# Kernel optimization log

Measured on AMD Instinct MI355X. Metric: run time of the kernel, lower is better.

The kernel has to match this reference:

```python
import jax, jax.numpy as jnp
import numpy as np

B, S, D = 1, 2048, 4096
H, KV = 32, 8
HD = D // H          # 128
N_REP = H // KV      # 4
ROPE_THETA = 10000.0


def setup_inputs() -> dict:
    key = jax.random.key(0)
    ks = jax.random.split(key, 5)
    x = jax.random.normal(ks[0], (B, S, D), dtype=jnp.float32)
    wq = jax.random.normal(ks[1], (H * HD, D), dtype=jnp.float32) * 0.02
    wk = jax.random.normal(ks[2], (KV * HD, D), dtype=jnp.float32) * 0.02
    wv = jax.random.normal(ks[3], (KV * HD, D), dtype=jnp.float32) * 0.02
    wo = jax.random.normal(ks[4], (D, H * HD), dtype=jnp.float32) * 0.02
    # precomputed RoPE frequencies: freqs_cis = exp(i * t * theta_j)
    inv_freq = 1.0 / (ROPE_THETA ** (np.arange(0, HD, 2, dtype=np.float32) / HD))  # [HD/2]
    angles = np.arange(S, dtype=np.float32)[:, None] * inv_freq[None, :]           # [S, HD/2]
    freqs_cos = jnp.asarray(np.cos(angles))
    freqs_sin = jnp.asarray(np.sin(angles))
    return {"x": x, "freqs_cos": freqs_cos, "freqs_sin": freqs_sin,
            "wq": wq, "wk": wk, "wv": wv, "wo": wo}


def _rope(t, cos, sin):
    # t: [B,S,h,HD]; even/odd interleaved pairs form complex numbers
    tr, ti = t[..., 0::2], t[..., 1::2]                 # [B,S,h,HD/2]
    cos = cos[None, :, None, :]
    sin = sin[None, :, None, :]
    out = jnp.stack([tr * cos - ti * sin, tr * sin + ti * cos], axis=-1)
    return out.reshape(t.shape)


def reference(x, freqs_cos, freqs_sin, wq, wk, wv, wo):
    bs, seqlen, _ = x.shape
    xq = jnp.einsum('bsd,ed->bse', x, wq).reshape(bs, seqlen, H, HD)
    xk = jnp.einsum('bsd,ed->bse', x, wk).reshape(bs, seqlen, KV, HD)
    xv = jnp.einsum('bsd,ed->bse', x, wv).reshape(bs, seqlen, KV, HD)
    xq = _rope(xq, freqs_cos, freqs_sin)
    xk = _rope(xk, freqs_cos, freqs_sin)
    # repeat_kv: GQA expand kv heads by n_rep
    keys = jnp.repeat(xk, N_REP, axis=2)    # [B,S,H,HD]
    values = jnp.repeat(xv, N_REP, axis=2)
    scale = 1.0 / np.sqrt(HD).astype(np.float32)
    scores = jnp.einsum('bshd,bthd->bhst', xq, keys) * scale  # [B,H,S,S]
    causal = jnp.tril(jnp.ones((seqlen, seqlen), dtype=bool))
    scores = jnp.where(causal[None, None], scores, jnp.finfo(scores.dtype).min)
    attn = jax.nn.softmax(scores, axis=-1)
    out = jnp.einsum('bhst,bthd->bshd', attn, values).reshape(bs, seqlen, H * HD)
    return jnp.einsum('bse,de->bsd', out, wo)
```

## Files before the change

### kernel.cpp

```cpp
#include <hip/hip_runtime.h>
#include <hip/hip_bf16.h>
#include <stdint.h>

#define SEQ   2048
#define DM    4096
#define NH    32
#define NKV   8
#define HD    128
#define DKV   1024

typedef __attribute__((ext_vector_type(8))) short bf8_t;
typedef __attribute__((ext_vector_type(4))) float f4_t;
typedef __attribute__((ext_vector_type(16))) float f16x;

__device__ __forceinline__ short f2bf(float f) {
  union { float f; uint32_t u; } v; v.f = f;
  uint32_t r = v.u + 0x7FFFu + ((v.u >> 16) & 1u);
  return (short)(r >> 16);
}
__device__ __forceinline__ float bf2f(short s) {
  union { uint32_t u; float f; } v; v.u = ((uint32_t)(uint16_t)s) << 16;
  return v.f;
}
__device__ __forceinline__ uint32_t cvtpk(float lo, float hi) {
  uint32_t r;
  asm("v_cvt_pk_bf16_f32 %0, %1, %2" : "=v"(r) : "v"(lo), "v"(hi));
  return r;
}

__device__ __forceinline__ void async_copy16(const void* gsrc, void* ldst) {
  auto g = reinterpret_cast<const __attribute__((address_space(1))) uint32_t*>(
      reinterpret_cast<uintptr_t>(gsrc));
  auto l = reinterpret_cast<__attribute__((address_space(3))) uint32_t*>(
      reinterpret_cast<uintptr_t>(ldst));
  __builtin_amdgcn_global_load_lds(g, l, 16, 0, 0);
}

__device__ __forceinline__ f4_t mfma16(bf8_t a, bf8_t b, f4_t c) {
  return __builtin_amdgcn_mfma_f32_16x16x32_bf16(a, b, c, 0, 0, 0);
}
__device__ __forceinline__ f16x mfma32(bf8_t a, bf8_t b, f16x c) {
  return __builtin_amdgcn_mfma_f32_32x32x16_bf16(a, b, c, 0, 0, 0);
}

__global__ void cvt_bf16_kernel(const float* __restrict__ in, short* __restrict__ out, int n4) {
  const int stride = gridDim.x * blockDim.x;
  for (int i = blockIdx.x * blockDim.x + threadIdx.x; i < n4; i += stride) {
    float4 v = ((const float4*)in)[i];
    short4 o;
    o.x = f2bf(v.x); o.y = f2bf(v.y); o.z = f2bf(v.z); o.w = f2bf(v.w);
    ((short4*)out)[i] = o;
  }
}

template<int MODE>
__global__ __launch_bounds__(256)
void gemm_bt_kernel(const short* __restrict__ A,
                    const short* __restrict__ Bq,
                    const short* __restrict__ Bk,
                    const short* __restrict__ Bv,
                    float* __restrict__ Cf,
                    short* __restrict__ Cq,
                    short* __restrict__ Ck,
                    short* __restrict__ Cv)
{
  __shared__ short Al[128 * 32];
  __shared__ short Bl[128 * 32];
  const int tid  = threadIdx.x;
  const int lane = tid & 63;
  const int wid  = tid >> 6;
  const int wr = wid >> 1, wc = wid & 1;
  const int row0 = blockIdx.y * 128;
  const int col0 = blockIdx.x * 128;

  const short* B; int bcol; int region = 0;
  if (MODE == 0) { B = Bq; bcol = col0; }
  else {
    if (col0 < DM)            { B = Bq; bcol = col0;             region = 0; }
    else if (col0 < DM + DKV) { B = Bk; bcol = col0 - DM;        region = 1; }
    else                      { B = Bv; bcol = col0 - DM - DKV;  region = 2; }
  }

  f4_t acc[4][4];
  #pragma unroll
  for (int i = 0; i < 4; i++)
    #pragma unroll
    for (int j = 0; j < 4; j++) { acc[i][j][0]=0.f; acc[i][j][1]=0.f; acc[i][j][2]=0.f; acc[i][j][3]=0.f; }

  const int cl = lane & 15, kh = lane >> 4;
  const int K = DM;

  for (int k0 = 0; k0 < K; k0 += 32) {
    #pragma unroll
    for (int i = 0; i < 2; ++i) {
      int c = tid + i * 256;
      async_copy16(&A[(size_t)(row0 + (c >> 2)) * K + k0 + (c & 3) * 8], &Al[c * 8]);
    }
    #pragma unroll
    for (int i = 0; i < 2; ++i) {
      int c = tid + i * 256;
      async_copy16(&B[(size_t)(bcol + (c >> 2)) * K + k0 + (c & 3) * 8], &Bl[c * 8]);
    }
    __syncthreads();

    bf8_t aF[4], bF[4];
    #pragma unroll
    for (int i = 0; i < 4; i++)
      aF[i] = *(const bf8_t*)&Al[(wr * 64 + i * 16 + cl) * 32 + kh * 8];
    #pragma unroll
    for (int i = 0; i < 4; i++)
      bF[i] = *(const bf8_t*)&Bl[(wc * 64 + i * 16 + cl) * 32 + kh * 8];

    #pragma unroll
    for (int mi = 0; mi < 4; mi++)
      #pragma unroll
      for (int ni = 0; ni < 4; ni++)
        acc[mi][ni] = mfma16(aF[mi], bF[ni], acc[mi][ni]);
    __syncthreads();
  }

  const int rb = kh * 4;
  #pragma unroll
  for (int mi = 0; mi < 4; mi++) {
    const int m0 = row0 + wr * 64 + mi * 16 + rb;
    #pragma unroll
    for (int ni = 0; ni < 4; ni++) {
      const int n = col0 + wc * 64 + ni * 16 + cl;
      if (MODE == 0) {
        #pragma unroll
        for (int r = 0; r < 4; r++) Cf[(size_t)(m0 + r) * DM + n] = acc[mi][ni][r];
      } else if (region == 0) {
        #pragma unroll
        for (int r = 0; r < 4; r++) Cq[(size_t)(m0 + r) * DM + n] = f2bf(acc[mi][ni][r]);
      } else if (region == 1) {
        const int nk = n - DM;
        #pragma unroll
        for (int r = 0; r < 4; r++) Ck[(size_t)(m0 + r) * DKV + nk] = f2bf(acc[mi][ni][r]);
      } else {
        const int nv = n - DM - DKV;
        short4 pk;
        pk.x = f2bf(acc[mi][ni][0]); pk.y = f2bf(acc[mi][ni][1]);
        pk.z = f2bf(acc[mi][ni][2]); pk.w = f2bf(acc[mi][ni][3]);
        *(short4*)&Cv[(size_t)nv * SEQ + m0] = pk;
      }
    }
  }
}

__global__ void rope_kernel(short* __restrict__ Qb, short* __restrict__ Kb,
                            const float* __restrict__ fcos, const float* __restrict__ fsin)
{
  const int NQP = SEQ * (DM / 2);
  const int NKP = SEQ * (DKV / 2);
  int idx = blockIdx.x * blockDim.x + threadIdx.x;
  if (idx >= NQP + NKP) return;
  short* T; int s, p, rowlen;
  if (idx < NQP) { T = Qb; s = idx >> 11; p = idx & 2047; rowlen = DM; }
  else { int j = idx - NQP; T = Kb; s = j >> 9; p = j & 511; rowlen = DKV; }
  const int h = p >> 6, i = p & 63;
  const float c  = fcos[s * 64 + i];
  const float sn = fsin[s * 64 + i];
  const size_t base = (size_t)s * rowlen + h * HD + 2 * i;
  const float e = bf2f(T[base]), o = bf2f(T[base + 1]);
  T[base]     = f2bf(e * c - o * sn);
  T[base + 1] = f2bf(e * sn + o * c);
}


__device__ __forceinline__ void flash_stage(const short* __restrict__ Kb,
                                            const short* __restrict__ Vt,
                                            short* Kl, short* Vl,
                                            int kv0, int hkv, int wid, int lane)
{
  #pragma unroll
  for (int i = 0; i < 4; ++i) {
    int c = wid * 256 + i * 64 + lane;
    int row = c >> 4, pos = c & 15;
    int dc = pos ^ (row & 7);
    async_copy16(&Kb[(size_t)(kv0 + row) * DKV + hkv * HD + dc * 8], &Kl[c * 8]);
  }
  #pragma unroll
  for (int i = 0; i < 4; ++i) {
    int c = wid * 256 + i * 64 + lane;
    int row = c >> 3, pos = c & 7;
    int kc = pos ^ (row & 7);
    async_copy16(&Vt[(size_t)(hkv * HD + row) * SEQ + kv0 + kc * 8], &Vl[c * 8]);
  }
}

union U4B8 { uint32_t w[4]; bf8_t v; };

__device__ __forceinline__ void flash_compute(const short* __restrict__ Kl,
                                              const short* __restrict__ Vl,
                                              const bf8_t* qF, f16x* accO,
                                              float& m_run, float& l_run,
                                              int kv0, int qw0, int c31, int hi)
{
  const float scale = 0.08838834764831845f;

  f16x accS[2];
  #pragma unroll
  for (int nu = 0; nu < 2; ++nu) {
    #pragma unroll
    for (int r = 0; r < 16; ++r) accS[nu][r] = 0.f;
  }
  #pragma unroll
  for (int nu = 0; nu < 2; ++nu) {
    const int row = nu * 32 + c31, rx = row & 7;
    #pragma unroll
    for (int s = 0; s < 8; ++s) {
      const int pos = (2 * s + hi) ^ rx;
      bf8_t kf = *(const bf8_t*)&Kl[row * 128 + pos * 8];
      accS[nu] = mfma32(kf, qF[s], accS[nu]);
    }
  }

  if (kv0 + 63 > qw0) {
    const int q_abs = qw0 + c31;
    #pragma unroll
    for (int nu = 0; nu < 2; ++nu)
      #pragma unroll
      for (int r = 0; r < 16; ++r) {
        const int kv_abs = kv0 + 32 * nu + (r & 3) + 8 * (r >> 2) + 4 * hi;
        if (kv_abs > q_abs) accS[nu][r] = -3.0e38f;
      }
  }

  float rm = -3.0e38f;
  #pragma unroll
  for (int nu = 0; nu < 2; ++nu)
    #pragma unroll
    for (int r = 0; r < 16; ++r) rm = fmaxf(rm, accS[nu][r]);
  rm = fmaxf(rm, __shfl_xor(rm, 32));
  const float pmax = rm * scale;
  if (!__all(pmax - m_run <= 8.0f)) {
    const float mnew = fmaxf(m_run, pmax);
    const float corr = __expf(m_run - mnew);
    m_run = mnew;
    l_run *= corr;
    #pragma unroll
    for (int dt = 0; dt < 4; ++dt)
      #pragma unroll
      for (int r = 0; r < 16; ++r) accO[dt][r] *= corr;
  }

  float tsum = 0.f;
  uint32_t u[8][2];
  #pragma unroll
  for (int m = 0; m < 8; ++m) {
    const int nu = m >> 2, rb = 4 * (m & 3);
    float p0 = __expf(fmaf(accS[nu][rb + 0], scale, -m_run));
    float p1 = __expf(fmaf(accS[nu][rb + 1], scale, -m_run));
    float p2 = __expf(fmaf(accS[nu][rb + 2], scale, -m_run));
    float p3 = __expf(fmaf(accS[nu][rb + 3], scale, -m_run));
    tsum += (p0 + p1) + (p2 + p3);
    u[m][0] = cvtpk(p0, p1);
    u[m][1] = cvtpk(p2, p3);
  }
  l_run += tsum + __shfl_xor(tsum, 32);

  bf8_t pa[4];
  #pragma unroll
  for (int ks = 0; ks < 4; ++ks) {
    const uint32_t a0 = u[2 * ks][0],     a1 = u[2 * ks][1];
    const uint32_t b0 = u[2 * ks + 1][0], b1 = u[2 * ks + 1][1];
    const uint32_t mp0 = hi ? a0 : b0, mp1 = hi ? a1 : b1;
    const uint32_t s0 = __shfl_xor(mp0, 32), s1 = __shfl_xor(mp1, 32);
    U4B8 f;
    f.w[0] = hi ? s0 : a0;
    f.w[1] = hi ? s1 : a1;
    f.w[2] = hi ? b0 : s0;
    f.w[3] = hi ? b1 : s1;
    pa[ks] = f.v;
  }

  #pragma unroll
  for (int dt = 0; dt < 4; ++dt) {
    const int row = dt * 32 + c31, rx = row & 7;
    #pragma unroll
    for (int ks = 0; ks < 4; ++ks) {
      const int pos = (2 * ks + hi) ^ rx;
      bf8_t vf = *(const bf8_t*)&Vl[row * 64 + pos * 8];
      accO[dt] = mfma32(vf, pa[ks], accO[dt]);
    }
  }
}

__global__ __launch_bounds__(256, 2)
void flash_kernel(const short* __restrict__ Qb,
                  const short* __restrict__ Kb,
                  const short* __restrict__ Vt,
                  short* __restrict__ Ob)
{
  __shared__ short Kl0[64 * 128], Kl1[64 * 128];
  __shared__ short Vl0[128 * 64], Vl1[128 * 64];

  const int tid = threadIdx.x, lane = tid & 63, wid = tid >> 6;
  const int c31 = lane & 31, hi = lane >> 5;

  const int b = blockIdx.x;
  const int pairid = b & 255, halfsel = b >> 8;
  const int h = pairid >> 3, p = pairid & 7;
  const int qt = halfsel ? (15 - p) : p;
  const int q0 = qt * 128;
  const int hkv = h >> 2;
  const int qw0 = q0 + wid * 32;

  bf8_t qF[8];
  {
    const size_t qb = (size_t)(qw0 + c31) * DM + h * HD + hi * 8;
    #pragma unroll
    for (int s = 0; s < 8; ++s) qF[s] = *(const bf8_t*)&Qb[qb + s * 16];
  }

  f16x accO[4];
  #pragma unroll
  for (int dt = 0; dt < 4; ++dt)
    #pragma unroll
    for (int r = 0; r < 16; ++r) accO[dt][r] = 0.f;
  float m_run = -INFINITY, l_run = 0.f;

  const int nt = (q0 >> 6) + 2;

  flash_stage(Kb, Vt, Kl0, Vl0, 0, hkv, wid, lane);
  __syncthreads();
  for (int t = 0; t < nt; t += 2) {
    flash_stage(Kb, Vt, Kl1, Vl1, (t + 1) * 64, hkv, wid, lane);
    if (t * 64 <= qw0 + 31)
      flash_compute(Kl0, Vl0, qF, accO, m_run, l_run, t * 64, qw0, c31, hi);
    __syncthreads();
    if (t + 2 < nt) flash_stage(Kb, Vt, Kl0, Vl0, (t + 2) * 64, hkv, wid, lane);
    if ((t + 1) * 64 <= qw0 + 31)
      flash_compute(Kl1, Vl1, qF, accO, m_run, l_run, (t + 1) * 64, qw0, c31, hi);
    __syncthreads();
  }

  short* Ol = (wid < 2) ? &Kl0[wid * 4096] : &Kl1[(wid - 2) * 4096];
  const float oinv = 1.0f / l_run;
  #pragma unroll
  for (int dt = 0; dt < 4; ++dt)
    #pragma unroll
    for (int w = 0; w < 8; ++w) {
      const int r = 2 * w;
      const int d0 = (r & 3) + 8 * (r >> 2) + 4 * hi + dt * 32;
      const uint32_t pk = cvtpk(accO[dt][r] * oinv, accO[dt][r + 1] * oinv);
      const int pos = (d0 >> 3) ^ (c31 & 7);
      *(uint32_t*)&Ol[c31 * 128 + pos * 8 + (d0 & 7)] = pk;
    }
  __syncthreads();
  const int rowq = lane >> 1;
  #pragma unroll
  for (int i = 0; i < 8; ++i) {
    const int dc = (lane & 1) * 8 + i;
    const int pos = dc ^ (rowq & 7);
    int4 v = *(const int4*)&Ol[rowq * 128 + pos * 8];
    *(int4*)&Ob[(size_t)(q0 + wid * 32 + rowq) * DM + h * HD + dc * 8] = v;
  }
}

extern "C" void kernel_launch(void* const* d_in, const int* in_sizes, int n_in,
                              void* d_out, int out_size, void* d_ws, size_t ws_size,
                              hipStream_t stream)
{
  const float* x    = (const float*)d_in[0];
  const float* fcos = (const float*)d_in[1];
  const float* fsin = (const float*)d_in[2];
  const float* wq   = (const float*)d_in[3];
  const float* wk   = (const float*)d_in[4];
  const float* wv   = (const float*)d_in[5];
  const float* wo   = (const float*)d_in[6];
  float* out = (float*)d_out;

  char* p = (char*)d_ws;
  short* xb  = (short*)p; p += (size_t)SEQ * DM * 2;
  short* wqb = (short*)p; p += (size_t)DM * DM * 2;
  short* wkb = (short*)p; p += (size_t)DKV * DM * 2;
  short* wvb = (short*)p; p += (size_t)DKV * DM * 2;
  short* wob = (short*)p; p += (size_t)DM * DM * 2;
  short* Qb  = (short*)p; p += (size_t)SEQ * DM * 2;
  short* Kb  = (short*)p; p += (size_t)SEQ * DKV * 2;
  short* Vt  = (short*)p; p += (size_t)DKV * SEQ * 2;
  short* Ab  = (short*)p; p += (size_t)SEQ * DM * 2;

  cvt_bf16_kernel<<<1024, 256, 0, stream>>>(x,  xb,  SEQ * DM / 4);
  cvt_bf16_kernel<<<2048, 256, 0, stream>>>(wq, wqb, DM * DM / 4);
  cvt_bf16_kernel<<<1024, 256, 0, stream>>>(wk, wkb, DKV * DM / 4);
  cvt_bf16_kernel<<<1024, 256, 0, stream>>>(wv, wvb, DKV * DM / 4);
  cvt_bf16_kernel<<<2048, 256, 0, stream>>>(wo, wob, DM * DM / 4);

  gemm_bt_kernel<1><<<dim3(48, 16), 256, 0, stream>>>(xb, wqb, wkb, wvb,
                                                      nullptr, Qb, Kb, Vt);
  rope_kernel<<<20480, 256, 0, stream>>>(Qb, Kb, fcos, fsin);
  flash_kernel<<<512, 256, 0, stream>>>(Qb, Kb, Vt, Ab);
  gemm_bt_kernel<0><<<dim3(32, 16), 256, 0, stream>>>(Ab, wob, nullptr, nullptr,
                                                      out, nullptr, nullptr, nullptr);
}
```

Before: 344.5 us.

## Replace GEMMs with double-buffered 8-wave 256-wide tiles and fuse fp32-to-bf16 conversions

```diff
diff --git a/kernel.cpp b/kernel.cpp
--- a/kernel.cpp
+++ b/kernel.cpp
@@ -43,89 +43,167 @@
   return __builtin_amdgcn_mfma_f32_32x32x16_bf16(a, b, c, 0, 0, 0);
 }
 
-__global__ void cvt_bf16_kernel(const float* __restrict__ in, short* __restrict__ out, int n4) {
+__global__ void cvt_all_kernel(const float* __restrict__ x,
+                               const float* __restrict__ wq,
+                               const float* __restrict__ wk,
+                               const float* __restrict__ wv,
+                               const float* __restrict__ wo,
+                               short* __restrict__ out)
+{
+  const int E0 = SEQ * DM / 4;
+  const int E1 = E0 + DM * DM / 4;
+  const int E2 = E1 + DKV * DM / 4;
+  const int E3 = E2 + DKV * DM / 4;
+  const int E4 = E3 + DM * DM / 4;
   const int stride = gridDim.x * blockDim.x;
-  for (int i = blockIdx.x * blockDim.x + threadIdx.x; i < n4; i += stride) {
-    float4 v = ((const float4*)in)[i];
+  for (int i = blockIdx.x * blockDim.x + threadIdx.x; i < E4; i += stride) {
+    const float4* src; int off;
+    if (i < E0)      { src = (const float4*)x;  off = i; }
+    else if (i < E1) { src = (const float4*)wq; off = i - E0; }
+    else if (i < E2) { src = (const float4*)wk; off = i - E1; }
+    else if (i < E3) { src = (const float4*)wv; off = i - E2; }
+    else             { src = (const float4*)wo; off = i - E3; }
+    float4 v = src[off];
     short4 o;
     o.x = f2bf(v.x); o.y = f2bf(v.y); o.z = f2bf(v.z); o.w = f2bf(v.w);
     ((short4*)out)[i] = o;
   }
 }
 
-template<int MODE>
-__global__ __launch_bounds__(256)
-void gemm_bt_kernel(const short* __restrict__ A,
-                    const short* __restrict__ Bq,
-                    const short* __restrict__ Bk,
-                    const short* __restrict__ Bv,
-                    float* __restrict__ Cf,
-                    short* __restrict__ Cq,
-                    short* __restrict__ Ck,
-                    short* __restrict__ Cv)
-{
-  __shared__ short Al[128 * 32];
-  __shared__ short Bl[128 * 32];
-  const int tid  = threadIdx.x;
-  const int lane = tid & 63;
-  const int wid  = tid >> 6;
-  const int wr = wid >> 1, wc = wid & 1;
-  const int row0 = blockIdx.y * 128;
-  const int col0 = blockIdx.x * 128;
-
-  const short* B; int bcol; int region = 0;
-  if (MODE == 0) { B = Bq; bcol = col0; }
+template<int MODE, int BM>
+__global__ __launch_bounds__(512, 2)
+void gemm8_kernel(const short* __restrict__ A,
+                  const short* __restrict__ Bq,
+                  const short* __restrict__ Bk,
+                  const short* __restrict__ Bv,
+                  float* __restrict__ Cf,
+                  short* __restrict__ Cq,
+                  short* __restrict__ Ck,
+                  short* __restrict__ Cv)
+{
+  constexpr int MREP = BM / 32;
+  constexpr int SPP  = MREP / 4;
+  constexpr int AJ   = BM / 128;
+  constexpr int NT   = DM / 64;
+
+  __shared__ short As[2][BM * 64];
+  __shared__ short Bs[2][256 * 64];
+
+  const int tid = threadIdx.x, lane = tid & 63, wid = tid >> 6;
+  const int wr = wid >> 2, wn = wid & 3;
+  const int cl = lane & 15, kh = lane >> 4;
+  const int row0 = blockIdx.y * BM;
+  const int col0 = blockIdx.x * 256;
+
+  const short* Bmat; int bcol; int region = 0;
+  if (MODE == 0) { Bmat = Bq; bcol = col0; }
   else {
-    if (col0 < DM)            { B = Bq; bcol = col0;             region = 0; }
-    else if (col0 < DM + DKV) { B = Bk; bcol = col0 - DM;        region = 1; }
-    else                      { B = Bv; bcol = col0 - DM - DKV;  region = 2; }
-  }
-
-  f4_t acc[4][4];
-  #pragma unroll
-  for (int i = 0; i < 4; i++)
+    if (col0 < DM)            { Bmat = Bq; bcol = col0;            region = 0; }
+    else if (col0 < DM + DKV) { Bmat = Bk; bcol = col0 - DM;       region = 1; }
+    else                      { Bmat = Bv; bcol = col0 - DM - DKV; region = 2; }
+  }
+
+  f4_t acc[MREP][4];
+  #pragma unroll
+  for (int i = 0; i < MREP; i++)
     #pragma unroll
     for (int j = 0; j < 4; j++) { acc[i][j][0]=0.f; acc[i][j][1]=0.f; acc[i][j][2]=0.f; acc[i][j][3]=0.f; }
 
-  const int cl = lane & 15, kh = lane >> 4;
-  const int K = DM;
-
-  for (int k0 = 0; k0 < K; k0 += 32) {
-    #pragma unroll
-    for (int i = 0; i < 2; ++i) {
-      int c = tid + i * 256;
-      async_copy16(&A[(size_t)(row0 + (c >> 2)) * K + k0 + (c & 3) * 8], &Al[c * 8]);
-    }
-    #pragma unroll
-    for (int i = 0; i < 2; ++i) {
-      int c = tid + i * 256;
-      async_copy16(&B[(size_t)(bcol + (c >> 2)) * K + k0 + (c & 3) * 8], &Bl[c * 8]);
-    }
-    __syncthreads();
-
-    bf8_t aF[4], bF[4];
-    #pragma unroll
-    for (int i = 0; i < 4; i++)
-      aF[i] = *(const bf8_t*)&Al[(wr * 64 + i * 16 + cl) * 32 + kh * 8];
-    #pragma unroll
-    for (int i = 0; i < 4; i++)
-      bF[i] = *(const bf8_t*)&Bl[(wc * 64 + i * 16 + cl) * 32 + kh * 8];
-
-    #pragma unroll
-    for (int mi = 0; mi < 4; mi++)
+  auto STGA = [&](short* T, int h, int kt) {
+    #pragma unroll
+    for (int j = 0; j < AJ; ++j) {
+      const int c = wid * (64 * AJ) + j * 64 + lane;
+      const int row = h * (BM / 2) + (c >> 3), pcol = c & 7;
+      const int lcol = pcol ^ (row & 7);
+      async_copy16(&A[(size_t)(row0 + row) * DM + kt * 64 + lcol * 8],
+                   &T[(h * (BM * 4) + c) * 8]);
+    }
+  };
+  auto STGB = [&](short* T, int h, int kt) {
+    #pragma unroll
+    for (int j = 0; j < 2; ++j) {
+      const int c = wid * 128 + j * 64 + lane;
+      const int row = h * 128 + (c >> 3), pcol = c & 7;
+      const int lcol = pcol ^ (row & 7);
+      async_copy16(&Bmat[(size_t)(bcol + row) * DM + kt * 64 + lcol * 8],
+                   &T[(h * 1024 + c) * 8]);
+    }
+  };
+
+  bf8_t bF[4][2];
+  bf8_t aF[SPP][2];
+  auto LDA = [&](const short* T, int ms0) {
+    #pragma unroll
+    for (int s = 0; s < SPP; ++s)
       #pragma unroll
-      for (int ni = 0; ni < 4; ni++)
-        acc[mi][ni] = mfma16(aF[mi], bF[ni], acc[mi][ni]);
-    __syncthreads();
-  }
+      for (int q = 0; q < 2; ++q) {
+        const int row = wr * (BM / 2) + (ms0 + s) * 16 + cl;
+        const int pcol = (q * 4 + kh) ^ (row & 7);
+        aF[s][q] = *(const bf8_t*)&T[(row * 8 + pcol) * 8];
+      }
+  };
+  auto LDB = [&](const short* T) {
+    #pragma unroll
+    for (int n = 0; n < 4; ++n)
+      #pragma unroll
+      for (int q = 0; q < 2; ++q) {
+        const int row = wn * 64 + n * 16 + cl;
+        const int pcol = (q * 4 + kh) ^ (row & 7);
+        bF[n][q] = *(const bf8_t*)&T[(row * 8 + pcol) * 8];
+      }
+  };
+
+#define PHASE(TA, TB, PH, READB, STGSTMT, VMC)                                \
+  {                                                                           \
+    LDA(TA, (PH) * SPP);                                                      \
+    if (READB) LDB(TB);                                                       \
+    STGSTMT                                                                   \
+    __builtin_amdgcn_s_barrier();                                             \
+    asm volatile("s_waitcnt lgkmcnt(0)" ::: "memory");                        \
+    __builtin_amdgcn_s_setprio(1);                                            \
+    _Pragma("unroll")                                                         \
+    for (int s_ = 0; s_ < SPP; ++s_) {                                        \
+      _Pragma("unroll")                                                       \
+      for (int n_ = 0; n_ < 4; ++n_) {                                        \
+        _Pragma("unroll")                                                     \
+        for (int q_ = 0; q_ < 2; ++q_)                                        \
+          acc[(PH) * SPP + s_][n_] =                                          \
+              mfma16(aF[s_][q_], bF[n_][q_], acc[(PH) * SPP + s_][n_]);       \
+      }                                                                       \
+    }                                                                         \
+    __builtin_amdgcn_s_setprio(0);                                            \
+    if (VMC) asm volatile("s_waitcnt vmcnt(4)" ::: "memory");                 \
+    __builtin_amdgcn_s_barrier();                                             \
+  }
+
+  STGB(Bs[0], 0, 0); STGB(Bs[0], 1, 0);
+  STGA(As[0], 0, 0); STGA(As[0], 1, 0);
+  STGB(Bs[1], 0, 1); STGB(Bs[1], 1, 1);
+  asm volatile("s_waitcnt vmcnt(4)" ::: "memory");
+  __builtin_amdgcn_s_barrier();
+
+  for (int i = 0; i < NT / 2; ++i) {
+    const int tA1 = 2 * i + 1;
+    int t2 = 2 * i + 2; if (t2 > NT - 1) t2 = NT - 1;
+    int t3 = 2 * i + 3; if (t3 > NT - 1) t3 = NT - 1;
+    PHASE(As[0], Bs[0], 0, true,  { STGA(As[1], 0, tA1); STGA(As[1], 1, tA1); }, false);
+    PHASE(As[0], Bs[0], 1, false, { STGB(Bs[0], 0, t2); }, false);
+    PHASE(As[0], Bs[0], 2, false, { STGB(Bs[0], 1, t2); }, false);
+    PHASE(As[0], Bs[0], 3, false, { }, true);
+    PHASE(As[1], Bs[1], 0, true,  { STGA(As[0], 0, t2); STGA(As[0], 1, t2); }, false);
+    PHASE(As[1], Bs[1], 1, false, { STGB(Bs[1], 0, t3); }, false);
+    PHASE(As[1], Bs[1], 2, false, { STGB(Bs[1], 1, t3); }, false);
+    PHASE(As[1], Bs[1], 3, false, { }, true);
+  }
+#undef PHASE
 
   const int rb = kh * 4;
   #pragma unroll
-  for (int mi = 0; mi < 4; mi++) {
-    const int m0 = row0 + wr * 64 + mi * 16 + rb;
+  for (int mi = 0; mi < MREP; mi++) {
+    const int m0 = row0 + wr * (BM / 2) + mi * 16 + rb;
     #pragma unroll
     for (int ni = 0; ni < 4; ni++) {
-      const int n = col0 + wc * 64 + ni * 16 + cl;
+      const int n = col0 + wn * 64 + ni * 16 + cl;
       if (MODE == 0) {
         #pragma unroll
         for (int r = 0; r < 4; r++) Cf[(size_t)(m0 + r) * DM + n] = acc[mi][ni][r];
@@ -166,7 +244,6 @@
   T[base + 1] = f2bf(e * sn + o * c);
 }
 
-
 __device__ __forceinline__ void flash_stage(const short* __restrict__ Kb,
                                             const short* __restrict__ Vt,
                                             short* Kl, short* Vl,
@@ -382,16 +459,12 @@
   short* Vt  = (short*)p; p += (size_t)DKV * SEQ * 2;
   short* Ab  = (short*)p; p += (size_t)SEQ * DM * 2;
 
-  cvt_bf16_kernel<<<1024, 256, 0, stream>>>(x,  xb,  SEQ * DM / 4);
-  cvt_bf16_kernel<<<2048, 256, 0, stream>>>(wq, wqb, DM * DM / 4);
-  cvt_bf16_kernel<<<1024, 256, 0, stream>>>(wk, wkb, DKV * DM / 4);
-  cvt_bf16_kernel<<<1024, 256, 0, stream>>>(wv, wvb, DKV * DM / 4);
-  cvt_bf16_kernel<<<2048, 256, 0, stream>>>(wo, wob, DM * DM / 4);
-
-  gemm_bt_kernel<1><<<dim3(48, 16), 256, 0, stream>>>(xb, wqb, wkb, wvb,
-                                                      nullptr, Qb, Kb, Vt);
+  cvt_all_kernel<<<2048, 256, 0, stream>>>(x, wq, wk, wv, wo, xb);
+
+  gemm8_kernel<1, 256><<<dim3(24, 8), 512, 0, stream>>>(xb, wqb, wkb, wvb,
+                                                        nullptr, Qb, Kb, Vt);
   rope_kernel<<<20480, 256, 0, stream>>>(Qb, Kb, fcos, fsin);
   flash_kernel<<<512, 256, 0, stream>>>(Qb, Kb, Vt, Ab);
-  gemm_bt_kernel<0><<<dim3(32, 16), 256, 0, stream>>>(Ab, wob, nullptr, nullptr,
-                                                      out, nullptr, nullptr, nullptr);
-}
+  gemm8_kernel<0, 128><<<dim3(16, 16), 512, 0, stream>>>(Ab, wob, nullptr, nullptr,
+                                                         out, nullptr, nullptr, nullptr);
+}
```

After: 289.8 us. -15.9%, faster.
